# Optimization experiments

Measured on AMD Instinct MI355X. Metric: run time of the kernel, lower is better.

The kernel has to match this reference:

```python
import jax, jax.numpy as jnp
import numpy as np

DIM = 16384
NOBS = 8192
EPS = 1e-20


def _soft(v, tau):
    return jnp.sign(v) * jnp.maximum(jnp.abs(v) - tau, 0.0)


def setup_inputs() -> dict:
    key = jax.random.key(0)
    ks = jax.random.split(key, 14)
    A = jax.random.normal(ks[0], (NOBS, DIM), jnp.float32) / np.float32(np.sqrt(DIM))
    b = jax.random.normal(ks[1], (NOBS,), jnp.float32)
    x_old = jax.random.normal(ks[2], (DIM,), jnp.float32)
    # soft-threshold to get a realistic sparse iterate (nontrivial zeros mask)
    x_cur = _soft(jax.random.normal(ks[3], (DIM,), jnp.float32), 0.5)
    mu = jnp.array([0.1], jnp.float32)
    smoothness = jnp.array([10.0], jnp.float32)

    def glorot(k, shape):
        return jax.random.normal(k, shape, jnp.float32) * np.float32(np.sqrt(2.0 / (shape[0] + shape[1])))

    W_u1 = glorot(ks[4], (20, 8))
    W_u2 = glorot(ks[5], (20, 20))
    W_u3 = glorot(ks[6], (20, 20))
    W_u4 = glorot(ks[7], (2, 20))
    W_s1 = glorot(ks[8], (30, 12))
    W_s2 = glorot(ks[9], (20, 30))
    W_s3 = glorot(ks[10], (10, 20))
    W_s4 = glorot(ks[11], (8, 10))
    return dict(x_old=x_old, x_cur=x_cur, A=A, b=b, mu=mu, smoothness=smoothness,
                W_u1=W_u1, W_u2=W_u2, W_u3=W_u3, W_u4=W_u4,
                W_s1=W_s1, W_s2=W_s2, W_s3=W_s3, W_s4=W_s4)


def reference(x_old, x_cur, A, b, mu, smoothness,
              W_u1, W_u2, W_u3, W_u4, W_s1, W_s2, W_s3, W_s4):
    L = smoothness[0]
    m = mu[0]

    def smooth(x):
        r = A @ x - b
        return 0.5 * jnp.dot(r, r)

    def nonsmooth(x):
        return m * jnp.sum(jnp.abs(x))

    smooth_loss = smooth(x_cur)
    old_smooth_loss = smooth(x_old)
    nonsmooth_loss = nonsmooth(x_cur)
    old_nonsmooth_loss = nonsmooth(x_old)
    loss = smooth_loss + nonsmooth_loss
    old_loss = old_smooth_loss + old_nonsmooth_loss

    zeros = (x_cur == 0).astype(x_cur.dtype)   # mask of zero coordinates
    non_zeros = 1.0 - zeros

    # normalized difference of iterates
    diff = x_cur - x_old
    diff_norm = jnp.linalg.norm(diff)
    diff = jnp.where(diff_norm > EPS, diff / diff_norm, diff)
    diff_zero = diff * zeros
    diff_nonzero = diff * non_zeros
    diff_zero_norm = diff_norm * jnp.linalg.norm(diff_zero)
    diff_nonzero_norm = diff_norm * jnp.linalg.norm(diff_nonzero)

    # normalized gradient of smooth part at current iterate
    grad = A.T @ (A @ x_cur - b)
    grad_norm = jnp.linalg.norm(grad)
    grad = jnp.where(grad_norm > EPS, grad / grad_norm, grad)
    grad_zero = grad * zeros
    grad_nonzero = grad * non_zeros
    grad_zero_norm = grad_norm * jnp.linalg.norm(grad_zero)
    grad_nonzero_norm = grad_norm * jnp.linalg.norm(grad_nonzero)

    # proximal-gradient residual (stopping criterion)
    prox = _soft(x_cur - grad_norm * grad / L, m / L)
    stop_vec = x_cur - prox
    stop_norm = jnp.linalg.norm(stop_vec)
    stop_vec = jnp.where(stop_norm > EPS, stop_vec / stop_norm, stop_vec)
    stop_zero = stop_vec * zeros
    stop_nonzero = stop_vec * non_zeros
    stop_zero_norm = stop_norm * jnp.linalg.norm(stop_zero)
    stop_nonzero_norm = stop_norm * jnp.linalg.norm(stop_nonzero)

    feats = jnp.stack([
        m,
        jnp.log1p(old_loss) - jnp.log1p(loss),
        jnp.log1p(old_smooth_loss) - jnp.log1p(smooth_loss),
        jnp.log1p(old_nonsmooth_loss) - jnp.log1p(nonsmooth_loss),
        jnp.log1p(grad_zero_norm),
        jnp.log1p(grad_nonzero_norm),
        jnp.log1p(diff_zero_norm),
        jnp.log1p(diff_nonzero_norm),
        jnp.log1p(stop_zero_norm),
        jnp.log1p(stop_nonzero_norm),
        jnp.dot(grad_zero, diff_zero),
        jnp.dot(grad_nonzero, diff_nonzero),
    ])  # (12,)

    # step-size MLP: 12 -> 30 -> 20 -> 10 -> 8, ReLU, no bias
    h = feats
    for W in (W_s1, W_s2, W_s3):
        h = jax.nn.relu(W @ h)
    alpha = W_s4 @ h  # (8,)

    # 1x1-conv stack == channel matmul on [8, dim]
    chans = jnp.stack([
        alpha[0] * grad_zero,
        alpha[1] * grad_nonzero,
        alpha[2] * stop_zero,
        alpha[3] * stop_nonzero,
        alpha[4] * diff_zero,
        alpha[5] * diff_nonzero,
        alpha[6] * grad_nonzero * diff_nonzero,
        alpha[7] * grad_zero * diff_zero,
    ])  # (8, dim)
    h2 = chans
    for W in (W_u1, W_u2, W_u3):
        h2 = jax.nn.relu(W @ h2)
    direction = W_u4 @ h2  # (2, dim)

    dir_1 = direction[0] * zeros
    dir_2 = direction[1] * non_zeros
    update = _soft(x_cur + (dir_1 - grad_norm * grad + diff_norm * dir_2) / L, m / L)
    return update
```

## Files before the change

### kernel.cpp

```cpp
#include <hip/hip_runtime.h>
#include <math.h>

#define DIM   16384
#define NOBS  8192
#define EPSN  1e-20f

__device__ __forceinline__ float softf(float v, float tau) {
    float a = fmaxf(fabsf(v) - tau, 0.0f);
    return copysignf(a, v);
}

__device__ __forceinline__ float dot4(float4 a, float4 b) {
    return a.x * b.x + a.y * b.y + a.z * b.z + a.w * b.w;
}

__device__ __forceinline__ float sum16(const float* p) {
    const float4* q = (const float4*)p;
    float4 s0 = q[0], s1 = q[1], s2 = q[2], s3 = q[3];
    float a = (s0.x + s0.y) + (s0.z + s0.w);
    float b = (s1.x + s1.y) + (s1.z + s1.w);
    float c = (s2.x + s2.y) + (s2.z + s2.w);
    float d = (s3.x + s3.y) + (s3.z + s3.w);
    return (a + b) + (c + d);
}

__global__ __launch_bounds__(1024) void k1_fused(
    const float* __restrict__ A, const float* __restrict__ xc,
    const float* __restrict__ xo, const float* __restrict__ b,
    float* __restrict__ ws_gp,
    float* __restrict__ ws_sc)
{
    const int t   = threadIdx.x;
    const int bid = blockIdx.x;
    __shared__ __align__(16) float redc[2][16];
    __shared__ __align__(16) float redo[2][16];
    __shared__ float bsh[32];

    const int row0 = bid * 32;
    if (t < 32) bsh[t] = b[row0 + t];

    const float4* xc4 = (const float4*)xc;
    const float4* xo4 = (const float4*)xo;

    float4 xcq[4], xoq[4], gpq[4];
#pragma unroll
    for (int k = 0; k < 4; ++k) {
        xcq[k] = xc4[k * 1024 + t];
        xoq[k] = xo4[k * 1024 + t];
        gpq[k] = make_float4(0.f, 0.f, 0.f, 0.f);
    }

    const float4* Arow = (const float4*)(A + (size_t)row0 * DIM);
    float4 acur[4], anxt[4];
#pragma unroll
    for (int k = 0; k < 4; ++k) acur[k] = Arow[k * 1024 + t];
    Arow += DIM / 4;

    float sum_r2 = 0.f, sum_ro2 = 0.f;
    __syncthreads();

    for (int r = 0; r < 32; ++r) {
        if (r < 31) {
#pragma unroll
            for (int k = 0; k < 4; ++k) anxt[k] = Arow[k * 1024 + t];
            Arow += DIM / 4;
        }

        float dc = 0.f, dn = 0.f;
#pragma unroll
        for (int k = 0; k < 4; ++k) {
            dc += dot4(acur[k], xcq[k]);
            dn += dot4(acur[k], xoq[k]);
        }
#pragma unroll
        for (int off = 32; off > 0; off >>= 1) {
            dc += __shfl_down(dc, off);
            dn += __shfl_down(dn, off);
        }
        if ((t & 63) == 0) {
            redc[r & 1][t >> 6] = dc;
            redo[r & 1][t >> 6] = dn;
        }
        __syncthreads();

        float rc = sum16(redc[r & 1]) - bsh[r];
        if (t == 0) sum_r2 += rc * rc;
        if (t == 1) {
            float ro = sum16(redo[r & 1]) - bsh[r];
            sum_ro2 += ro * ro;
        }
#pragma unroll
        for (int k = 0; k < 4; ++k) {
            gpq[k].x += acur[k].x * rc;
            gpq[k].y += acur[k].y * rc;
            gpq[k].z += acur[k].z * rc;
            gpq[k].w += acur[k].w * rc;
        }
        if (r < 31) {
#pragma unroll
            for (int k = 0; k < 4; ++k) acur[k] = anxt[k];
        }
    }

    float4* gp4 = (float4*)(ws_gp + (size_t)bid * DIM);
#pragma unroll
    for (int k = 0; k < 4; ++k) gp4[k * 1024 + t] = gpq[k];
    if (t == 0) ws_sc[bid * 2 + 0] = sum_r2;
    if (t == 1) ws_sc[bid * 2 + 1] = sum_ro2;
}

__global__ __launch_bounds__(256) void k2a(
    const float* __restrict__ ws_gp, float* __restrict__ ws_gp2)
{
    const int t     = threadIdx.x;
    const int chunk = blockIdx.x & 63;
    const int s     = blockIdx.x >> 6;
    const int j     = chunk * 256 + t;

    const float* base = ws_gp + (size_t)s * 64 * DIM + j;
    float acc[4] = {0.f, 0.f, 0.f, 0.f};
#pragma unroll
    for (int pp = 0; pp < 16; ++pp) {
#pragma unroll
        for (int q = 0; q < 4; ++q)
            acc[q] += base[(size_t)(pp * 4 + q) * DIM];
    }
    ws_gp2[s * DIM + j] = (acc[0] + acc[1]) + (acc[2] + acc[3]);
}

__global__ __launch_bounds__(256) void k2b(
    const float* __restrict__ ws_gp2, const float* __restrict__ xc,
    const float* __restrict__ xo, const float* __restrict__ mu,
    const float* __restrict__ sm,
    float* __restrict__ grad, float* __restrict__ ws_red)
{
    const int t = threadIdx.x;
    const int j = blockIdx.x * 256 + t;

    float g = (ws_gp2[j] + ws_gp2[DIM + j]) + (ws_gp2[2 * DIM + j] + ws_gp2[3 * DIM + j]);
    grad[j] = g;

    const float x  = xc[j];
    const float xv = xo[j];
    const float z  = (x == 0.f) ? 1.f : 0.f;
    const float nz = 1.f - z;
    const float d  = x - xv;
    const float m = mu[0], L = sm[0];
    const float invL = 1.f / L;
    const float pv = softf(x - g * invL, m * invL);
    const float sv = x - pv;

    float vals[10];
    vals[0] = g * g * z;
    vals[1] = g * g * nz;
    vals[2] = d * d * z;
    vals[3] = d * d * nz;
    vals[4] = g * d * z;
    vals[5] = g * d * nz;
    vals[6] = fabsf(x);
    vals[7] = fabsf(xv);
    vals[8] = sv * sv * z;
    vals[9] = sv * sv * nz;

    __shared__ float s[40];
#pragma unroll
    for (int k = 0; k < 10; ++k) {
#pragma unroll
        for (int off = 32; off > 0; off >>= 1) vals[k] += __shfl_down(vals[k], off);
    }
    if ((t & 63) == 0) {
#pragma unroll
        for (int k = 0; k < 10; ++k) s[(t >> 6) * 10 + k] = vals[k];
    }
    __syncthreads();
    if (t < 10)
        ws_red[blockIdx.x * 10 + t] = (s[t] + s[10 + t]) + (s[20 + t] + s[30 + t]);
}

__device__ __forceinline__ float blockReduce256(float v, float* sh) {
    const int t = threadIdx.x;
#pragma unroll
    for (int off = 32; off > 0; off >>= 1) v += __shfl_down(v, off);
    __syncthreads();
    if ((t & 63) == 0) sh[t >> 6] = v;
    __syncthreads();
    return sh[0] + sh[1] + sh[2] + sh[3];
}

__global__ __launch_bounds__(256) void k3_scalars(
    const float* __restrict__ ws_sc,
    const float* __restrict__ ws_red,
    const float* __restrict__ mu,
    const float* __restrict__ Ws1, const float* __restrict__ Ws2,
    const float* __restrict__ Ws3, const float* __restrict__ Ws4,
    float* __restrict__ ws_out)
{
    const int t = threadIdx.x;
    __shared__ float sh[4];
    __shared__ float feats[12];
    __shared__ float ba[32], bb[32];
    __shared__ float snorms[3];

    float sum_r2  = blockReduce256(ws_sc[2 * t + 0], sh);
    float sum_ro2 = blockReduce256(ws_sc[2 * t + 1], sh);

    float red10[10];
#pragma unroll
    for (int k = 0; k < 10; ++k) {
        float v = (t < 64) ? ws_red[t * 10 + k] : 0.f;
        red10[k] = blockReduce256(v, sh);
    }
    const float gz2 = red10[0], gnz2 = red10[1], dz2 = red10[2], dnz2 = red10[3];
    const float gdz = red10[4], gdnz = red10[5], sxc = red10[6], sxo = red10[7];
    const float svz2 = red10[8], svnz2 = red10[9];

    if (t == 0) {
        const float grad_norm = sqrtf(gz2 + gnz2);
        const float diff_norm = sqrtf(dz2 + dnz2);
        const float stop_norm = sqrtf(svz2 + svnz2);
        const float m = mu[0];
        float smooth = 0.5f * sum_r2, old_smooth = 0.5f * sum_ro2;
        float nonsm = m * sxc, old_nonsm = m * sxo;
        float loss = smooth + nonsm, old_loss = old_smooth + old_nonsm;

        float fg = (grad_norm > EPSN) ? 1.f / grad_norm : 1.f;
        float fd = (diff_norm > EPSN) ? 1.f / diff_norm : 1.f;
        float fs = (stop_norm > EPSN) ? 1.f / stop_norm : 1.f;

        feats[0]  = m;
        feats[1]  = log1pf(old_loss) - log1pf(loss);
        feats[2]  = log1pf(old_smooth) - log1pf(smooth);
        feats[3]  = log1pf(old_nonsm) - log1pf(nonsm);
        feats[4]  = log1pf(grad_norm * fg * sqrtf(gz2));
        feats[5]  = log1pf(grad_norm * fg * sqrtf(gnz2));
        feats[6]  = log1pf(diff_norm * fd * sqrtf(dz2));
        feats[7]  = log1pf(diff_norm * fd * sqrtf(dnz2));
        feats[8]  = log1pf(stop_norm * fs * sqrtf(svz2));
        feats[9]  = log1pf(stop_norm * fs * sqrtf(svnz2));
        feats[10] = gdz  * fg * fd;
        feats[11] = gdnz * fg * fd;
        snorms[0] = grad_norm; snorms[1] = diff_norm; snorms[2] = stop_norm;
    }
    __syncthreads();

    if (t < 30) {
        float s0 = 0.f;
#pragma unroll
        for (int j = 0; j < 12; ++j) s0 += Ws1[t * 12 + j] * feats[j];
        ba[t] = fmaxf(s0, 0.f);
    }
    __syncthreads();
    if (t < 20) {
        float s0 = 0.f;
#pragma unroll
        for (int j = 0; j < 30; ++j) s0 += Ws2[t * 30 + j] * ba[j];
        bb[t] = fmaxf(s0, 0.f);
    }
    __syncthreads();
    if (t < 10) {
        float s0 = 0.f;
#pragma unroll
        for (int j = 0; j < 20; ++j) s0 += Ws3[t * 20 + j] * bb[j];
        ba[t] = fmaxf(s0, 0.f);
    }
    __syncthreads();
    if (t < 8) {
        float s0 = 0.f;
#pragma unroll
        for (int j = 0; j < 10; ++j) s0 += Ws4[t * 10 + j] * ba[j];
        ws_out[t] = s0;
    }
    if (t == 0) {
        ws_out[8]  = snorms[0];
        ws_out[9]  = snorms[1];
        ws_out[10] = snorms[2];
    }
}

__global__ __launch_bounds__(256) void k4_update(
    const float* __restrict__ grad, const float* __restrict__ xc,
    const float* __restrict__ xo, const float* __restrict__ mu,
    const float* __restrict__ sm, const float* __restrict__ ws_out,
    const float* __restrict__ Wu1, const float* __restrict__ Wu2,
    const float* __restrict__ Wu3, const float* __restrict__ Wu4,
    float* __restrict__ out)
{
    __shared__ float w1[160], w2[400], w3[400], w4[40];
    const int t = threadIdx.x;
    for (int i = t; i < 160; i += 256) w1[i] = Wu1[i];
    for (int i = t; i < 400; i += 256) w2[i] = Wu2[i];
    for (int i = t; i < 400; i += 256) w3[i] = Wu3[i];
    if (t < 40) w4[t] = Wu4[t];
    __syncthreads();

    const int j = blockIdx.x * 256 + t;
    const float m = mu[0], L = sm[0];
    const float invL = 1.f / L;
    const float gn = ws_out[8], dn = ws_out[9], sn = ws_out[10];
    float a[8];
#pragma unroll
    for (int k = 0; k < 8; ++k) a[k] = ws_out[k];

    const float g  = grad[j];
    const float x  = xc[j];
    const float xv = xo[j];
    const float z  = (x == 0.f) ? 1.f : 0.f;
    const float nz = 1.f - z;

    const float fg = (gn > EPSN) ? 1.f / gn : 1.f;
    const float fd = (dn > EPSN) ? 1.f / dn : 1.f;
    const float fs = (sn > EPSN) ? 1.f / sn : 1.f;
    const float gg = (gn > EPSN) ? g : gn * g;

    const float pv = softf(x - gg * invL, m * invL);
    const float sv = x - pv;

    const float gN = g * fg;
    const float dN = (x - xv) * fd;
    const float sN = sv * fs;

    float ch[8];
    ch[0] = a[0] * gN * z;
    ch[1] = a[1] * gN * nz;
    ch[2] = a[2] * sN * z;
    ch[3] = a[3] * sN * nz;
    ch[4] = a[4] * dN * z;
    ch[5] = a[5] * dN * nz;
    ch[6] = a[6] * (gN * nz) * (dN * nz);
    ch[7] = a[7] * (gN * z) * (dN * z);

    float h1[20];
#pragma unroll
    for (int i = 0; i < 20; ++i) {
        float s0 = 0.f;
#pragma unroll
        for (int k = 0; k < 8; ++k) s0 += w1[i * 8 + k] * ch[k];
        h1[i] = fmaxf(s0, 0.f);
    }
    float h2[20];
#pragma unroll
    for (int i = 0; i < 20; ++i) {
        float s0 = 0.f;
#pragma unroll
        for (int k = 0; k < 20; ++k) s0 += w2[i * 20 + k] * h1[k];
        h2[i] = fmaxf(s0, 0.f);
    }
    float h3[20];
#pragma unroll
    for (int i = 0; i < 20; ++i) {
        float s0 = 0.f;
#pragma unroll
        for (int k = 0; k < 20; ++k) s0 += w3[i * 20 + k] * h2[k];
        h3[i] = fmaxf(s0, 0.f);
    }
    float d0 = 0.f, d1 = 0.f;
#pragma unroll
    for (int k = 0; k < 20; ++k) {
        d0 += w4[k] * h3[k];
        d1 += w4[20 + k] * h3[k];
    }

    const float dir1 = d0 * z;
    const float dir2 = d1 * nz;
    const float arg  = x + (dir1 - gg + dn * dir2) * invL;
    out[j] = softf(arg, m * invL);
}

extern "C" void kernel_launch(void* const* d_in, const int* in_sizes, int n_in,
                              void* d_out, int out_size, void* d_ws, size_t ws_size,
                              hipStream_t stream)
{
    const float* x_old = (const float*)d_in[0];
    const float* x_cur = (const float*)d_in[1];
    const float* A     = (const float*)d_in[2];
    const float* b     = (const float*)d_in[3];
    const float* mu    = (const float*)d_in[4];
    const float* sm    = (const float*)d_in[5];
    const float* Wu1   = (const float*)d_in[6];
    const float* Wu2   = (const float*)d_in[7];
    const float* Wu3   = (const float*)d_in[8];
    const float* Wu4   = (const float*)d_in[9];
    const float* Ws1   = (const float*)d_in[10];
    const float* Ws2   = (const float*)d_in[11];
    const float* Ws3   = (const float*)d_in[12];
    const float* Ws4   = (const float*)d_in[13];
    float* out = (float*)d_out;

    float* ws       = (float*)d_ws;
    float* ws_gp    = ws;
    float* ws_sc    = ws_gp  + (size_t)256 * DIM;
    float* ws_gp2   = ws_sc  + 512;
    float* ws_red   = ws_gp2 + 4 * DIM;
    float* ws_grad  = ws_red + 640;
    float* ws_alpha = ws_grad + DIM;

    k1_fused <<<256, 1024, 0, stream>>>(A, x_cur, x_old, b, ws_gp, ws_sc);
    k2a      <<<256, 256,  0, stream>>>(ws_gp, ws_gp2);
    k2b      <<<64,  256,  0, stream>>>(ws_gp2, x_cur, x_old, mu, sm, ws_grad, ws_red);
    k3_scalars<<<1,  256,  0, stream>>>(ws_sc, ws_red, mu, Ws1, Ws2, Ws3, Ws4, ws_alpha);
    k4_update<<<64,  256,  0, stream>>>(ws_grad, x_cur, x_old, mu, sm, ws_alpha,
                                        Wu1, Wu2, Wu3, Wu4, out);
}
```

Baseline: 134.4 us.

## Fuse partial-sum reduction kernels and merge scalar MLP into update kernel

The k2a and k2b kernels become one 1024-thread kernel that reduces the per-block gradient partials through shared memory. The scalar-feature MLP kernel is merged into the update kernel, so every block redundantly recomputes the 12 global reductions and the small step-size MLP, which drops two launches and a global round-trip. In k1, the main loop switches to two-row double buffering with a raw s_barrier that waits only on LDS, so global prefetches stay in flight across the barrier. The cost is redundant per-block scalar work and a reduction that uses fewer blocks.

```diff
diff --git a/kernel.cpp b/kernel.cpp
--- a/kernel.cpp
+++ b/kernel.cpp
@@ -49,58 +49,62 @@
         xoq[k] = xo4[k * 1024 + t];
         gpq[k] = make_float4(0.f, 0.f, 0.f, 0.f);
     }
-
-    const float4* Arow = (const float4*)(A + (size_t)row0 * DIM);
-    float4 acur[4], anxt[4];
-#pragma unroll
-    for (int k = 0; k < 4; ++k) acur[k] = Arow[k * 1024 + t];
-    Arow += DIM / 4;
+    __syncthreads();
+
+    const float4* Abase = (const float4*)A + (size_t)row0 * (DIM / 4);
+    float4 b0q[4], b1q[4];
+#pragma unroll
+    for (int k = 0; k < 4; ++k) b0q[k] = Abase[k * 1024 + t];
+#pragma unroll
+    for (int k = 0; k < 4; ++k) b1q[k] = Abase[(DIM / 4) + k * 1024 + t];
 
     float sum_r2 = 0.f, sum_ro2 = 0.f;
-    __syncthreads();
-
-    for (int r = 0; r < 32; ++r) {
-        if (r < 31) {
-#pragma unroll
-            for (int k = 0; k < 4; ++k) anxt[k] = Arow[k * 1024 + t];
-            Arow += DIM / 4;
-        }
-
-        float dc = 0.f, dn = 0.f;
-#pragma unroll
-        for (int k = 0; k < 4; ++k) {
-            dc += dot4(acur[k], xcq[k]);
-            dn += dot4(acur[k], xoq[k]);
-        }
-#pragma unroll
-        for (int off = 32; off > 0; off >>= 1) {
-            dc += __shfl_down(dc, off);
-            dn += __shfl_down(dn, off);
-        }
-        if ((t & 63) == 0) {
-            redc[r & 1][t >> 6] = dc;
-            redo[r & 1][t >> 6] = dn;
-        }
-        __syncthreads();
-
-        float rc = sum16(redc[r & 1]) - bsh[r];
-        if (t == 0) sum_r2 += rc * rc;
-        if (t == 1) {
-            float ro = sum16(redo[r & 1]) - bsh[r];
-            sum_ro2 += ro * ro;
-        }
-#pragma unroll
-        for (int k = 0; k < 4; ++k) {
-            gpq[k].x += acur[k].x * rc;
-            gpq[k].y += acur[k].y * rc;
-            gpq[k].z += acur[k].z * rc;
-            gpq[k].w += acur[k].w * rc;
-        }
-        if (r < 31) {
-#pragma unroll
-            for (int k = 0; k < 4; ++k) acur[k] = anxt[k];
-        }
-    }
+
+#define K1_BODY(ROW, BQ, PAR)                                                  \
+    do {                                                                       \
+        float dc = 0.f, dn = 0.f;                                              \
+        _Pragma("unroll")                                                      \
+        for (int k = 0; k < 4; ++k) {                                          \
+            dc += dot4(BQ[k], xcq[k]);                                         \
+            dn += dot4(BQ[k], xoq[k]);                                         \
+        }                                                                      \
+        _Pragma("unroll")                                                      \
+        for (int off = 32; off > 0; off >>= 1) {                               \
+            dc += __shfl_down(dc, off);                                        \
+            dn += __shfl_down(dn, off);                                        \
+        }                                                                      \
+        if ((t & 63) == 0) {                                                   \
+            redc[PAR][t >> 6] = dc;                                            \
+            redo[PAR][t >> 6] = dn;                                            \
+        }                                                                      \
+        asm volatile("s_waitcnt lgkmcnt(0)" ::: "memory");                     \
+        __builtin_amdgcn_s_barrier();                                          \
+        asm volatile("" ::: "memory");                                         \
+        float rc = sum16(redc[PAR]) - bsh[ROW];                                \
+        if (t == 0) sum_r2 += rc * rc;                                         \
+        if (t == 1) {                                                          \
+            float ro = sum16(redo[PAR]) - bsh[ROW];                            \
+            sum_ro2 += ro * ro;                                                \
+        }                                                                      \
+        _Pragma("unroll")                                                      \
+        for (int k = 0; k < 4; ++k) {                                          \
+            gpq[k].x += BQ[k].x * rc;                                          \
+            gpq[k].y += BQ[k].y * rc;                                          \
+            gpq[k].z += BQ[k].z * rc;                                          \
+            gpq[k].w += BQ[k].w * rc;                                          \
+        }                                                                      \
+        if ((ROW) + 2 < 32) {                                                  \
+            const float4* An = Abase + (size_t)((ROW) + 2) * (DIM / 4);        \
+            _Pragma("unroll")                                                  \
+            for (int k = 0; k < 4; ++k) BQ[k] = An[k * 1024 + t];              \
+        }                                                                      \
+    } while (0)
+
+    for (int rr = 0; rr < 32; rr += 2) {
+        K1_BODY(rr,     b0q, 0);
+        K1_BODY(rr + 1, b1q, 1);
+    }
+#undef K1_BODY
 
     float4* gp4 = (float4*)(ws_gp + (size_t)bid * DIM);
 #pragma unroll
@@ -109,112 +113,126 @@
     if (t == 1) ws_sc[bid * 2 + 1] = sum_ro2;
 }
 
-__global__ __launch_bounds__(256) void k2a(
-    const float* __restrict__ ws_gp, float* __restrict__ ws_gp2)
-{
-    const int t     = threadIdx.x;
-    const int chunk = blockIdx.x & 63;
-    const int s     = blockIdx.x >> 6;
-    const int j     = chunk * 256 + t;
-
-    const float* base = ws_gp + (size_t)s * 64 * DIM + j;
-    float acc[4] = {0.f, 0.f, 0.f, 0.f};
-#pragma unroll
-    for (int pp = 0; pp < 16; ++pp) {
-#pragma unroll
-        for (int q = 0; q < 4; ++q)
-            acc[q] += base[(size_t)(pp * 4 + q) * DIM];
-    }
-    ws_gp2[s * DIM + j] = (acc[0] + acc[1]) + (acc[2] + acc[3]);
-}
-
-__global__ __launch_bounds__(256) void k2b(
-    const float* __restrict__ ws_gp2, const float* __restrict__ xc,
+__global__ __launch_bounds__(1024) void k2_fused(
+    const float* __restrict__ ws_gp, const float* __restrict__ xc,
     const float* __restrict__ xo, const float* __restrict__ mu,
     const float* __restrict__ sm,
     float* __restrict__ grad, float* __restrict__ ws_red)
 {
     const int t = threadIdx.x;
-    const int j = blockIdx.x * 256 + t;
-
-    float g = (ws_gp2[j] + ws_gp2[DIM + j]) + (ws_gp2[2 * DIM + j] + ws_gp2[3 * DIM + j]);
-    grad[j] = g;
-
-    const float x  = xc[j];
-    const float xv = xo[j];
-    const float z  = (x == 0.f) ? 1.f : 0.f;
-    const float nz = 1.f - z;
-    const float d  = x - xv;
-    const float m = mu[0], L = sm[0];
-    const float invL = 1.f / L;
-    const float pv = softf(x - g * invL, m * invL);
-    const float sv = x - pv;
-
-    float vals[10];
-    vals[0] = g * g * z;
-    vals[1] = g * g * nz;
-    vals[2] = d * d * z;
-    vals[3] = d * d * nz;
-    vals[4] = g * d * z;
-    vals[5] = g * d * nz;
-    vals[6] = fabsf(x);
-    vals[7] = fabsf(xv);
-    vals[8] = sv * sv * z;
-    vals[9] = sv * sv * nz;
-
-    __shared__ float s[40];
-#pragma unroll
-    for (int k = 0; k < 10; ++k) {
-#pragma unroll
-        for (int off = 32; off > 0; off >>= 1) vals[k] += __shfl_down(vals[k], off);
-    }
-    if ((t & 63) == 0) {
-#pragma unroll
-        for (int k = 0; k < 10; ++k) s[(t >> 6) * 10 + k] = vals[k];
+    const int s = t >> 8;
+    const int c = t & 255;
+    const int j = blockIdx.x * 256 + c;
+
+    __shared__ float sums[4][256];
+    __shared__ float sred[4][10];
+
+    const float* base = ws_gp + (size_t)(s * 64) * DIM + j;
+    float a0 = 0.f, a1 = 0.f, a2 = 0.f, a3 = 0.f;
+#pragma unroll
+    for (int i = 0; i < 16; ++i) {
+        a0 += base[(size_t)(4 * i + 0) * DIM];
+        a1 += base[(size_t)(4 * i + 1) * DIM];
+        a2 += base[(size_t)(4 * i + 2) * DIM];
+        a3 += base[(size_t)(4 * i + 3) * DIM];
+    }
+    sums[s][c] = (a0 + a1) + (a2 + a3);
+    __syncthreads();
+
+    if (t < 256) {
+        const int jj = blockIdx.x * 256 + t;
+        float g = (sums[0][t] + sums[1][t]) + (sums[2][t] + sums[3][t]);
+        grad[jj] = g;
+
+        const float x  = xc[jj];
+        const float xv = xo[jj];
+        const float z  = (x == 0.f) ? 1.f : 0.f;
+        const float nz = 1.f - z;
+        const float d  = x - xv;
+        const float m = mu[0], L = sm[0];
+        const float invL = 1.f / L;
+        const float pv = softf(x - g * invL, m * invL);
+        const float sv = x - pv;
+
+        float vals[10];
+        vals[0] = g * g * z;
+        vals[1] = g * g * nz;
+        vals[2] = d * d * z;
+        vals[3] = d * d * nz;
+        vals[4] = g * d * z;
+        vals[5] = g * d * nz;
+        vals[6] = fabsf(x);
+        vals[7] = fabsf(xv);
+        vals[8] = sv * sv * z;
+        vals[9] = sv * sv * nz;
+
+#pragma unroll
+        for (int k = 0; k < 10; ++k) {
+#pragma unroll
+            for (int off = 32; off > 0; off >>= 1)
+                vals[k] += __shfl_down(vals[k], off);
+        }
+        if ((t & 63) == 0) {
+#pragma unroll
+            for (int k = 0; k < 10; ++k) sred[t >> 6][k] = vals[k];
+        }
     }
     __syncthreads();
     if (t < 10)
-        ws_red[blockIdx.x * 10 + t] = (s[t] + s[10 + t]) + (s[20 + t] + s[30 + t]);
-}
-
-__device__ __forceinline__ float blockReduce256(float v, float* sh) {
-    const int t = threadIdx.x;
-#pragma unroll
-    for (int off = 32; off > 0; off >>= 1) v += __shfl_down(v, off);
-    __syncthreads();
-    if ((t & 63) == 0) sh[t >> 6] = v;
-    __syncthreads();
-    return sh[0] + sh[1] + sh[2] + sh[3];
-}
-
-__global__ __launch_bounds__(256) void k3_scalars(
+        ws_red[blockIdx.x * 10 + t] =
+            (sred[0][t] + sred[1][t]) + (sred[2][t] + sred[3][t]);
+}
+
+__global__ __launch_bounds__(256) void k34_update(
     const float* __restrict__ ws_sc,
     const float* __restrict__ ws_red,
-    const float* __restrict__ mu,
+    const float* __restrict__ grad, const float* __restrict__ xc,
+    const float* __restrict__ xo, const float* __restrict__ mu,
+    const float* __restrict__ sm,
     const float* __restrict__ Ws1, const float* __restrict__ Ws2,
     const float* __restrict__ Ws3, const float* __restrict__ Ws4,
-    float* __restrict__ ws_out)
+    const float* __restrict__ Wu1, const float* __restrict__ Wu2,
+    const float* __restrict__ Wu3, const float* __restrict__ Wu4,
+    float* __restrict__ out)
 {
-    const int t = threadIdx.x;
-    __shared__ float sh[4];
+    __shared__ float w1[160], w2[400], w3[400], w4[40];
+    __shared__ float sred[4][12];
     __shared__ float feats[12];
     __shared__ float ba[32], bb[32];
-    __shared__ float snorms[3];
-
-    float sum_r2  = blockReduce256(ws_sc[2 * t + 0], sh);
-    float sum_ro2 = blockReduce256(ws_sc[2 * t + 1], sh);
-
-    float red10[10];
-#pragma unroll
-    for (int k = 0; k < 10; ++k) {
-        float v = (t < 64) ? ws_red[t * 10 + k] : 0.f;
-        red10[k] = blockReduce256(v, sh);
-    }
-    const float gz2 = red10[0], gnz2 = red10[1], dz2 = red10[2], dnz2 = red10[3];
-    const float gdz = red10[4], gdnz = red10[5], sxc = red10[6], sxo = red10[7];
-    const float svz2 = red10[8], svnz2 = red10[9];
+    __shared__ float alpha_sh[12];
+
+    const int t = threadIdx.x;
+    for (int i = t; i < 160; i += 256) w1[i] = Wu1[i];
+    for (int i = t; i < 400; i += 256) w2[i] = Wu2[i];
+    for (int i = t; i < 400; i += 256) w3[i] = Wu3[i];
+    if (t < 40) w4[t] = Wu4[t];
+
+    float v[12];
+    v[0] = ws_sc[2 * t + 0];
+    v[1] = ws_sc[2 * t + 1];
+#pragma unroll
+    for (int k = 0; k < 10; ++k) v[2 + k] = (t < 64) ? ws_red[t * 10 + k] : 0.f;
+#pragma unroll
+    for (int k = 0; k < 12; ++k) {
+#pragma unroll
+        for (int off = 32; off > 0; off >>= 1) v[k] += __shfl_down(v[k], off);
+    }
+    if ((t & 63) == 0) {
+#pragma unroll
+        for (int k = 0; k < 12; ++k) sred[t >> 6][k] = v[k];
+    }
+    __syncthreads();
 
     if (t == 0) {
+        float r[12];
+#pragma unroll
+        for (int k = 0; k < 12; ++k)
+            r[k] = (sred[0][k] + sred[1][k]) + (sred[2][k] + sred[3][k]);
+        const float sum_r2 = r[0], sum_ro2 = r[1];
+        const float gz2 = r[2], gnz2 = r[3], dz2 = r[4], dnz2 = r[5];
+        const float gdz = r[6], gdnz = r[7], sxc = r[8], sxo = r[9];
+        const float svz2 = r[10], svnz2 = r[11];
+
         const float grad_norm = sqrtf(gz2 + gnz2);
         const float diff_norm = sqrtf(dz2 + dnz2);
         const float stop_norm = sqrtf(svz2 + svnz2);
@@ -239,67 +257,48 @@
         feats[9]  = log1pf(stop_norm * fs * sqrtf(svnz2));
         feats[10] = gdz  * fg * fd;
         feats[11] = gdnz * fg * fd;
-        snorms[0] = grad_norm; snorms[1] = diff_norm; snorms[2] = stop_norm;
+        alpha_sh[8]  = grad_norm;
+        alpha_sh[9]  = diff_norm;
+        alpha_sh[10] = stop_norm;
     }
     __syncthreads();
 
     if (t < 30) {
         float s0 = 0.f;
 #pragma unroll
-        for (int j = 0; j < 12; ++j) s0 += Ws1[t * 12 + j] * feats[j];
+        for (int k = 0; k < 12; ++k) s0 += Ws1[t * 12 + k] * feats[k];
         ba[t] = fmaxf(s0, 0.f);
     }
     __syncthreads();
     if (t < 20) {
         float s0 = 0.f;
 #pragma unroll
-        for (int j = 0; j < 30; ++j) s0 += Ws2[t * 30 + j] * ba[j];
+        for (int k = 0; k < 30; ++k) s0 += Ws2[t * 30 + k] * ba[k];
         bb[t] = fmaxf(s0, 0.f);
     }
     __syncthreads();
     if (t < 10) {
         float s0 = 0.f;
 #pragma unroll
-        for (int j = 0; j < 20; ++j) s0 += Ws3[t * 20 + j] * bb[j];
+        for (int k = 0; k < 20; ++k) s0 += Ws3[t * 20 + k] * bb[k];
         ba[t] = fmaxf(s0, 0.f);
     }
     __syncthreads();
     if (t < 8) {
         float s0 = 0.f;
 #pragma unroll
-        for (int j = 0; j < 10; ++j) s0 += Ws4[t * 10 + j] * ba[j];
-        ws_out[t] = s0;
-    }
-    if (t == 0) {
-        ws_out[8]  = snorms[0];
-        ws_out[9]  = snorms[1];
-        ws_out[10] = snorms[2];
-    }
-}
-
-__global__ __launch_bounds__(256) void k4_update(
-    const float* __restrict__ grad, const float* __restrict__ xc,
-    const float* __restrict__ xo, const float* __restrict__ mu,
-    const float* __restrict__ sm, const float* __restrict__ ws_out,
-    const float* __restrict__ Wu1, const float* __restrict__ Wu2,
-    const float* __restrict__ Wu3, const float* __restrict__ Wu4,
-    float* __restrict__ out)
-{
-    __shared__ float w1[160], w2[400], w3[400], w4[40];
-    const int t = threadIdx.x;
-    for (int i = t; i < 160; i += 256) w1[i] = Wu1[i];
-    for (int i = t; i < 400; i += 256) w2[i] = Wu2[i];
-    for (int i = t; i < 400; i += 256) w3[i] = Wu3[i];
-    if (t < 40) w4[t] = Wu4[t];
+        for (int k = 0; k < 10; ++k) s0 += Ws4[t * 10 + k] * ba[k];
+        alpha_sh[t] = s0;
+    }
     __syncthreads();
 
     const int j = blockIdx.x * 256 + t;
     const float m = mu[0], L = sm[0];
     const float invL = 1.f / L;
-    const float gn = ws_out[8], dn = ws_out[9], sn = ws_out[10];
+    const float gn = alpha_sh[8], dn = alpha_sh[9], sn = alpha_sh[10];
     float a[8];
 #pragma unroll
-    for (int k = 0; k < 8; ++k) a[k] = ws_out[k];
+    for (int k = 0; k < 8; ++k) a[k] = alpha_sh[k];
 
     const float g  = grad[j];
     const float x  = xc[j];
@@ -386,18 +385,14 @@
     const float* Ws4   = (const float*)d_in[13];
     float* out = (float*)d_out;
 
-    float* ws       = (float*)d_ws;
-    float* ws_gp    = ws;
-    float* ws_sc    = ws_gp  + (size_t)256 * DIM;
-    float* ws_gp2   = ws_sc  + 512;
-    float* ws_red   = ws_gp2 + 4 * DIM;
-    float* ws_grad  = ws_red + 640;
-    float* ws_alpha = ws_grad + DIM;
-
-    k1_fused <<<256, 1024, 0, stream>>>(A, x_cur, x_old, b, ws_gp, ws_sc);
-    k2a      <<<256, 256,  0, stream>>>(ws_gp, ws_gp2);
-    k2b      <<<64,  256,  0, stream>>>(ws_gp2, x_cur, x_old, mu, sm, ws_grad, ws_red);
-    k3_scalars<<<1,  256,  0, stream>>>(ws_sc, ws_red, mu, Ws1, Ws2, Ws3, Ws4, ws_alpha);
-    k4_update<<<64,  256,  0, stream>>>(ws_grad, x_cur, x_old, mu, sm, ws_alpha,
-                                        Wu1, Wu2, Wu3, Wu4, out);
-}
+    float* ws      = (float*)d_ws;
+    float* ws_gp   = ws;
+    float* ws_sc   = ws_gp  + (size_t)256 * DIM;
+    float* ws_red  = ws_sc  + 512;
+    float* ws_grad = ws_red + 640;
+
+    k1_fused  <<<256, 1024, 0, stream>>>(A, x_cur, x_old, b, ws_gp, ws_sc);
+    k2_fused  <<<64,  1024, 0, stream>>>(ws_gp, x_cur, x_old, mu, sm, ws_grad, ws_red);
+    k34_update<<<64,  256,  0, stream>>>(ws_sc, ws_red, ws_grad, x_cur, x_old, mu, sm,
+                                         Ws1, Ws2, Ws3, Ws4, Wu1, Wu2, Wu3, Wu4, out);
+}
```

After: 330.6 us. +146.0%, slower.
